# Kernel optimization log

Hardware: AMD Instinct MI355X
Metric: run time of the kernel (lower is better)

Reference implementation:

```python
import jax, jax.numpy as jnp
import numpy as np

NUM_CLASSES = 9
B, H, W = 8, 768, 768


def setup_inputs() -> dict:
    key = jax.random.key(0)
    k1, k2 = jax.random.split(key)
    masks = jax.random.randint(k1, (B, H, W), 0, NUM_CLASSES, dtype=jnp.int32)
    outputs = jax.random.normal(k2, (B, NUM_CLASSES, H, W), dtype=jnp.float32)
    return {"masks": masks, "outputs": outputs}


def reference(masks, outputs):
    b, c, h, w = outputs.shape
    k = NUM_CLASSES
    eye = jnp.eye(k, dtype=outputs.dtype)
    smooth = eye * 0.9 + (1.0 - eye) * (0.1 / 8.0)  # [K, K] smoothed targets

    # Fused segment-mean over all pixels: segment id = batch*K + class label.
    feats = jnp.transpose(outputs, (0, 2, 3, 1)).reshape(b * h * w, c)  # [BHW, C]
    ids = (jnp.arange(b, dtype=jnp.int32)[:, None, None] * k + masks).reshape(-1)
    sums = jax.ops.segment_sum(feats, ids, num_segments=b * k).reshape(b, k, c)
    counts = jax.ops.segment_sum(
        jnp.ones((b * h * w,), outputs.dtype), ids, num_segments=b * k
    ).reshape(b, k)

    # torch.unique(mask)[1:] drops label 0 (background); mask absent classes.
    protos = sums[:, 1:, :] / jnp.maximum(counts[:, 1:, None], 1.0)  # [B, K-1, C]
    present = counts[:, 1:] > 0  # [B, K-1]

    logp = jax.nn.log_softmax(protos, axis=-1)  # [B, K-1, C]
    tgt = smooth[1:]  # [K-1, C] soft targets for classes 1..K-1
    per_proto = -jnp.sum(tgt[None, :, :] * logp, axis=-1)  # [B, K-1]

    n_present = jnp.maximum(jnp.sum(present).astype(outputs.dtype), 1.0)
    loss = jnp.sum(jnp.where(present, per_proto, 0.0)) / n_present
    return loss
```

## Files before the change

### kernel.cpp

```cpp
#include <hip/hip_runtime.h>
#include <math.h>

#define NB 8
#define NC 9
#define PIXELS (768*768)
#define BLOCK 256
#define PPT 8
#define CHUNK_PX (BLOCK * PPT)
#define NCHUNK (PIXELS / CHUNK_PX)
#define NITER (PPT / 4)
#define NWAVE (BLOCK / 64)
#define GRID (NB * NCHUNK)
#define SLOT 80

__device__ __forceinline__ float butterfly8(const float s[8], int p, int q, int r)
{
    float u[4];
    #pragma unroll
    for (int j = 0; j < 4; ++j) {
        float x = p ? s[j] : s[j + 4];
        float y = __shfl_xor(x, 1, 64);
        u[j] = (p ? s[j + 4] : s[j]) + y;
    }
    float v2[2];
    #pragma unroll
    for (int j = 0; j < 2; ++j) {
        float x = q ? u[j] : u[j + 2];
        float y = __shfl_xor(x, 2, 64);
        v2[j] = (q ? u[j + 2] : u[j]) + y;
    }
    float w;
    {
        float x = r ? v2[0] : v2[1];
        float y = __shfl_xor(x, 4, 64);
        w = (r ? v2[1] : v2[0]) + y;
    }
    w += __shfl_xor(w, 8, 64);
    w += __shfl_xor(w, 16, 64);
    w += __shfl_xor(w, 32, 64);
    return w;
}

__global__ __launch_bounds__(BLOCK, 4)
void accum_kernel(const int* __restrict__ masks,
                  const float* __restrict__ outputs,
                  float* __restrict__ partial)
{
    int blk = blockIdx.x;
    int chunk = blk % NCHUNK;
    int b = blk / NCHUNK;
    int t = threadIdx.x;
    int wave = t >> 6;
    int lane = t & 63;

    const int4* __restrict__ m4 =
        (const int4*)(masks + (size_t)b * PIXELS + (size_t)chunk * CHUNK_PX);
    int4 m[NITER];
    #pragma unroll
    for (int i = 0; i < NITER; ++i) m[i] = m4[t + i * BLOCK];

    float fm[PPT][8];
    #pragma unroll
    for (int i = 0; i < NITER; ++i) {
        int mv[4] = { m[i].x, m[i].y, m[i].z, m[i].w };
        #pragma unroll
        for (int e = 0; e < 4; ++e) {
            #pragma unroll
            for (int k = 0; k < 8; ++k)
                fm[i * 4 + e][k] = (mv[e] == k + 1) ? 1.0f : 0.0f;
        }
    }

    __shared__ float red[NC][NWAVE][8];
    __shared__ float red_c[NWAVE][8];

    const int p = lane & 1;
    const int q = (lane >> 1) & 1;
    const int r = (lane >> 2) & 1;

    {
        float cnt[8];
        #pragma unroll
        for (int k = 0; k < 8; ++k) cnt[k] = 0.f;
        #pragma unroll
        for (int e = 0; e < PPT; ++e) {
            #pragma unroll
            for (int k = 0; k < 8; ++k) cnt[k] += fm[e][k];
        }
        float w = butterfly8(cnt, p, q, r);
        if (lane < 8) red_c[wave][(p << 2) | (q << 1) | r] = w;
    }

    const float* outbase = outputs + (size_t)b * NC * PIXELS + (size_t)chunk * CHUNK_PX;

    #pragma unroll
    for (int c = 0; c < NC; ++c) {
        const float4* o4 = (const float4*)(outbase + (size_t)c * PIXELS);
        float4 buf[NITER];
        #pragma unroll
        for (int i = 0; i < NITER; ++i) buf[i] = o4[t + i * BLOCK];

        float s[8];
        #pragma unroll
        for (int k = 0; k < 8; ++k) s[k] = 0.f;

        #pragma unroll
        for (int i = 0; i < NITER; ++i) {
            float v[4] = { buf[i].x, buf[i].y, buf[i].z, buf[i].w };
            #pragma unroll
            for (int e = 0; e < 4; ++e) {
                #pragma unroll
                for (int k = 0; k < 8; ++k)
                    s[k] = fmaf(fm[i * 4 + e][k], v[e], s[k]);
            }
        }

        float w = butterfly8(s, p, q, r);
        if (lane < 8) red[c][wave][(p << 2) | (q << 1) | r] = w;
    }

    __syncthreads();

    if (t < NC * 8) {
        int c = t >> 3;
        int k = t & 7;
        float tot = 0.f;
        #pragma unroll
        for (int w = 0; w < NWAVE; ++w) tot += red[c][w][k];
        partial[(size_t)blk * SLOT + c * 8 + k] = tot;
    } else if (t < NC * 8 + 8) {
        int k = t - NC * 8;
        float tot = 0.f;
        #pragma unroll
        for (int w = 0; w < NWAVE; ++w) tot += red_c[w][k];
        partial[(size_t)blk * SLOT + 72 + k] = tot;
    }
}

__global__ __launch_bounds__(1024)
void finalize_kernel(const float* __restrict__ partial,
                     float* __restrict__ out)
{
    __shared__ float tot[NB][SLOT];
    int t = threadIdx.x;

    if (t < NB * SLOT) {
        int b = t / SLOT;
        int col = t % SLOT;
        const float* p = partial + (size_t)b * NCHUNK * SLOT + col;
        float s = 0.f;
        #pragma unroll 8
        for (int blk = 0; blk < NCHUNK; ++blk) s += p[(size_t)blk * SLOT];
        tot[b][col] = s;
    }
    __syncthreads();

    if (t < 64) {
        int b = t >> 3;
        int cls = t & 7;

        float cntv = tot[b][72 + cls];
        float denom = fmaxf(cntv, 1.0f);

        float pr[NC];
        float mx = -INFINITY;
        #pragma unroll
        for (int c = 0; c < NC; ++c) {
            pr[c] = tot[b][c * 8 + cls] / denom;
            mx = fmaxf(mx, pr[c]);
        }
        float se = 0.f;
        #pragma unroll
        for (int c = 0; c < NC; ++c) se += expf(pr[c] - mx);
        float lse = logf(se);

        float per = 0.f;
        #pragma unroll
        for (int c = 0; c < NC; ++c) {
            float tgt = (c == cls + 1) ? 0.9f : 0.0125f;
            per -= tgt * (pr[c] - mx - lse);
        }

        bool present = cntv > 0.f;
        float val = present ? per : 0.f;
        float np  = present ? 1.f : 0.f;
        #pragma unroll
        for (int off = 32; off > 0; off >>= 1) {
            val += __shfl_down(val, off, 64);
            np  += __shfl_down(np,  off, 64);
        }
        if (t == 0) out[0] = val / fmaxf(np, 1.f);
    }
}

extern "C" void kernel_launch(void* const* d_in, const int* in_sizes, int n_in,
                              void* d_out, int out_size, void* d_ws, size_t ws_size,
                              hipStream_t stream) {
    const int*   masks   = (const int*)d_in[0];
    const float* outputs = (const float*)d_in[1];
    float* partial = (float*)d_ws;

    accum_kernel<<<GRID, BLOCK, 0, stream>>>(masks, outputs, partial);
    finalize_kernel<<<1, 1024, 0, stream>>>(partial, (float*)d_out);
}
```

Baseline: 257.4 us.

## Split finalize into per-batch parallel reduction and use nontemporal streaming loads

The main accumulation kernel now reads the mask and logit streams with nontemporal loads, so single-use data bypasses cache retention. The single-block finalize is split into a reduce kernel with one block per batch, where threads stride the chunk partials three ways, and a tiny 64-thread loss kernel. This spreads the serial partial reduction across more CUs but adds an extra kernel launch and a round trip through workspace memory.

```diff
diff --git a/kernel.cpp b/kernel.cpp
--- a/kernel.cpp
+++ b/kernel.cpp
@@ -12,6 +12,10 @@
 #define NWAVE (BLOCK / 64)
 #define GRID (NB * NCHUNK)
 #define SLOT 80
+#define ROWSPLIT 3
+
+typedef float f32x4 __attribute__((ext_vector_type(4)));
+typedef int   i32x4 __attribute__((ext_vector_type(4)));
 
 __device__ __forceinline__ float butterfly8(const float s[8], int p, int q, int r)
 {
@@ -53,21 +57,21 @@
     int wave = t >> 6;
     int lane = t & 63;
 
-    const int4* __restrict__ m4 =
-        (const int4*)(masks + (size_t)b * PIXELS + (size_t)chunk * CHUNK_PX);
-    int4 m[NITER];
-    #pragma unroll
-    for (int i = 0; i < NITER; ++i) m[i] = m4[t + i * BLOCK];
+    const i32x4* __restrict__ m4 =
+        (const i32x4*)(masks + (size_t)b * PIXELS + (size_t)chunk * CHUNK_PX);
+    i32x4 m[NITER];
+    #pragma unroll
+    for (int i = 0; i < NITER; ++i) m[i] = __builtin_nontemporal_load(m4 + t + i * BLOCK);
 
     float fm[PPT][8];
     #pragma unroll
     for (int i = 0; i < NITER; ++i) {
-        int mv[4] = { m[i].x, m[i].y, m[i].z, m[i].w };
         #pragma unroll
         for (int e = 0; e < 4; ++e) {
+            int mv = m[i][e];
             #pragma unroll
             for (int k = 0; k < 8; ++k)
-                fm[i * 4 + e][k] = (mv[e] == k + 1) ? 1.0f : 0.0f;
+                fm[i * 4 + e][k] = (mv == k + 1) ? 1.0f : 0.0f;
         }
     }
 
@@ -95,10 +99,10 @@
 
     #pragma unroll
     for (int c = 0; c < NC; ++c) {
-        const float4* o4 = (const float4*)(outbase + (size_t)c * PIXELS);
-        float4 buf[NITER];
-        #pragma unroll
-        for (int i = 0; i < NITER; ++i) buf[i] = o4[t + i * BLOCK];
+        const f32x4* o4 = (const f32x4*)(outbase + (size_t)c * PIXELS);
+        f32x4 buf[NITER];
+        #pragma unroll
+        for (int i = 0; i < NITER; ++i) buf[i] = __builtin_nontemporal_load(o4 + t + i * BLOCK);
 
         float s[8];
         #pragma unroll
@@ -106,12 +110,12 @@
 
         #pragma unroll
         for (int i = 0; i < NITER; ++i) {
-            float v[4] = { buf[i].x, buf[i].y, buf[i].z, buf[i].w };
             #pragma unroll
             for (int e = 0; e < 4; ++e) {
+                float v = buf[i][e];
                 #pragma unroll
                 for (int k = 0; k < 8; ++k)
-                    s[k] = fmaf(fm[i * 4 + e][k], v[e], s[k]);
+                    s[k] = fmaf(fm[i * 4 + e][k], v, s[k]);
             }
         }
 
@@ -137,60 +141,69 @@
     }
 }
 
-__global__ __launch_bounds__(1024)
-void finalize_kernel(const float* __restrict__ partial,
-                     float* __restrict__ out)
-{
-    __shared__ float tot[NB][SLOT];
+__global__ __launch_bounds__(256)
+void reduce_kernel(const float* __restrict__ partial,
+                   float* __restrict__ tot)
+{
+    int b = blockIdx.x;
     int t = threadIdx.x;
-
-    if (t < NB * SLOT) {
-        int b = t / SLOT;
+    __shared__ float acc[ROWSPLIT][SLOT];
+
+    if (t < SLOT * ROWSPLIT) {
         int col = t % SLOT;
+        int rg  = t / SLOT;
         const float* p = partial + (size_t)b * NCHUNK * SLOT + col;
         float s = 0.f;
         #pragma unroll 8
-        for (int blk = 0; blk < NCHUNK; ++blk) s += p[(size_t)blk * SLOT];
-        tot[b][col] = s;
+        for (int row = rg; row < NCHUNK; row += ROWSPLIT)
+            s += __builtin_nontemporal_load(p + (size_t)row * SLOT);
+        acc[rg][col] = s;
     }
     __syncthreads();
 
-    if (t < 64) {
-        int b = t >> 3;
-        int cls = t & 7;
-
-        float cntv = tot[b][72 + cls];
-        float denom = fmaxf(cntv, 1.0f);
-
-        float pr[NC];
-        float mx = -INFINITY;
-        #pragma unroll
-        for (int c = 0; c < NC; ++c) {
-            pr[c] = tot[b][c * 8 + cls] / denom;
-            mx = fmaxf(mx, pr[c]);
-        }
-        float se = 0.f;
-        #pragma unroll
-        for (int c = 0; c < NC; ++c) se += expf(pr[c] - mx);
-        float lse = logf(se);
-
-        float per = 0.f;
-        #pragma unroll
-        for (int c = 0; c < NC; ++c) {
-            float tgt = (c == cls + 1) ? 0.9f : 0.0125f;
-            per -= tgt * (pr[c] - mx - lse);
-        }
-
-        bool present = cntv > 0.f;
-        float val = present ? per : 0.f;
-        float np  = present ? 1.f : 0.f;
-        #pragma unroll
-        for (int off = 32; off > 0; off >>= 1) {
-            val += __shfl_down(val, off, 64);
-            np  += __shfl_down(np,  off, 64);
-        }
-        if (t == 0) out[0] = val / fmaxf(np, 1.f);
-    }
+    if (t < SLOT)
+        tot[(size_t)b * SLOT + t] = acc[0][t] + acc[1][t] + acc[2][t];
+}
+
+__global__ __launch_bounds__(64)
+void final_kernel(const float* __restrict__ tot,
+                  float* __restrict__ out)
+{
+    int t = threadIdx.x;
+    int b = t >> 3;
+    int cls = t & 7;
+
+    float cntv = tot[(size_t)b * SLOT + 72 + cls];
+    float denom = fmaxf(cntv, 1.0f);
+
+    float pr[NC];
+    float mx = -INFINITY;
+    #pragma unroll
+    for (int c = 0; c < NC; ++c) {
+        pr[c] = tot[(size_t)b * SLOT + c * 8 + cls] / denom;
+        mx = fmaxf(mx, pr[c]);
+    }
+    float se = 0.f;
+    #pragma unroll
+    for (int c = 0; c < NC; ++c) se += expf(pr[c] - mx);
+    float lse = logf(se);
+
+    float per = 0.f;
+    #pragma unroll
+    for (int c = 0; c < NC; ++c) {
+        float tgt = (c == cls + 1) ? 0.9f : 0.0125f;
+        per -= tgt * (pr[c] - mx - lse);
+    }
+
+    bool present = cntv > 0.f;
+    float val = present ? per : 0.f;
+    float np  = present ? 1.f : 0.f;
+    #pragma unroll
+    for (int off = 32; off > 0; off >>= 1) {
+        val += __shfl_down(val, off, 64);
+        np  += __shfl_down(np,  off, 64);
+    }
+    if (t == 0) out[0] = val / fmaxf(np, 1.f);
 }
 
 extern "C" void kernel_launch(void* const* d_in, const int* in_sizes, int n_in,
@@ -199,7 +212,9 @@
     const int*   masks   = (const int*)d_in[0];
     const float* outputs = (const float*)d_in[1];
     float* partial = (float*)d_ws;
+    float* tot     = (float*)((char*)d_ws + 768 * 1024);
 
     accum_kernel<<<GRID, BLOCK, 0, stream>>>(masks, outputs, partial);
-    finalize_kernel<<<1, 1024, 0, stream>>>(partial, (float*)d_out);
-}
+    reduce_kernel<<<NB, 256, 0, stream>>>(partial, tot);
+    final_kernel<<<1, 64, 0, stream>>>(tot, (float*)d_out);
+}
```

Measured after the change: 238.7 us. 1.08x faster.
